# Optimization experiments

Hardware: AMD Instinct MI355X
Metric: run time of the kernel (lower is better)

Reference implementation:

```python
import jax, jax.numpy as jnp
import numpy as np

P2 = 8
BN_EPS = 1e-5


def _slice_maps(p2):
    # Faithfully reproduce the buggy fs[:, i*j-1] indexing: later loop
    # iterations overwrite earlier ones; slots never written stay zero.
    last = {}
    for i in range(1, p2 + 1):
        for j in range(1, p2 + 1):
            last[i * j - 1] = (i - 1, j - 1)
    src_i = np.zeros(p2 * p2, np.int32)
    src_j = np.zeros(p2 * p2, np.int32)
    mask = np.zeros(p2 * p2, np.float32)
    for k, (ii, jj) in last.items():
        src_i[k], src_j[k], mask[k] = ii, jj, 1.0
    # unslice: output patch (i,j) reads slot (i+1)*(j+1)-1
    uns = np.array([[(i + 1) * (j + 1) - 1 for j in range(p2)] for i in range(p2)], np.int32)
    return src_i, src_j, mask, uns


def setup_inputs() -> dict:
    key = jax.random.key(0)
    ks = jax.random.split(key, 16)
    C, N, p2 = 32, 8, P2
    s = 0.05
    inp = {
        "x": jax.random.normal(ks[0], (8, C, 512, 512), jnp.float32),
        "w30": jax.random.normal(ks[1], (N, C, 3, 3), jnp.float32) * s,
        "b30": jnp.zeros((N,), jnp.float32),
        "w10": jax.random.normal(ks[2], (C, C), jnp.float32) * s,
        "b10": jnp.zeros((C,), jnp.float32),
        "w11": jax.random.normal(ks[3], (N, N), jnp.float32) * s,
        "b11": jnp.zeros((N,), jnp.float32),
        "w12a": jax.random.normal(ks[4], (p2, p2 * p2), jnp.float32) * s,
        "b12a": jnp.zeros((p2,), jnp.float32),
        "w12b": jax.random.normal(ks[5], (p2, p2), jnp.float32) * s,
        "b12b": jnp.zeros((p2,), jnp.float32),
        "w12c": jax.random.normal(ks[6], (p2 * p2, p2), jnp.float32) * s,
        "b12c": jnp.zeros((p2 * p2,), jnp.float32),
        "w31": jax.random.normal(ks[7], (C, C), jnp.float32) * s,
        "b31": jnp.zeros((C,), jnp.float32),
        "bn_gamma": jnp.ones((C,), jnp.float32),
        "bn_beta": jnp.zeros((C,), jnp.float32),
        "bn_mean": jnp.zeros((C,), jnp.float32),
        "bn_var": jnp.ones((C,), jnp.float32),
    }
    return inp


def reference(x, w30, b30, w10, b10, w11, b11, w12a, b12a, w12b, b12b,
              w12c, b12c, w31, b31, bn_gamma, bn_beta, bn_mean, bn_var):
    p2 = P2
    b, C, H, W = x.shape
    h, wd = H // p2, W // p2
    L = h * wd
    N = w30.shape[0]
    src_i, src_j, mask_np, uns = _slice_maps(p2)

    # --- slice into patches (with the original's overwrite/zero semantics) ---
    patches = x.reshape(b, C, p2, h, p2, wd).transpose(0, 2, 4, 1, 3, 5)  # [b,p2,p2,C,h,w]
    fs = patches[:, src_i, src_j] * jnp.asarray(mask_np)[None, :, None, None, None]
    fs = fs.reshape(b * p2 * p2, C, h, wd)

    # --- graph_convolution ---
    B = jax.lax.conv_general_dilated(fs, w30, (1, 1), 'SAME',
            dimension_numbers=('NCHW', 'OIHW', 'NCHW')) + b30[None, :, None, None]
    B = jax.nn.relu(B)                                    # [bp, N, h, w]
    B1 = B.reshape(b * p2 * p2, N, L)
    fs1 = fs.reshape(b * p2 * p2, C, L)
    fs2 = jnp.einsum('bnl,bcl->bnc', B1, fs1)              # [bp, N, C]
    fs3 = jax.nn.relu(jnp.einsum('on,bnc->boc', w11, fs2) + b11[None, :, None])
    fs5 = jax.nn.relu(jnp.einsum('oc,bcn->bon', w10, fs3.transpose(0, 2, 1)) + b10[None, :, None])  # [bp,C,N]
    fs6 = jnp.einsum('bnl,bcn->bcl', B1, fs5)              # [bp, C, L]
    fs6 = fs6.reshape(b, p2 * p2, C, h, wd)

    fg = x.reshape(b, C, 8, H // 8, 8, W // 8).mean(axis=(3, 5))  # [b,C,8,8]
    fg1 = fg.reshape(b, C, p2 * p2).transpose(0, 2, 1)            # [b, p2^2, C]
    g = jax.nn.relu(jnp.einsum('ok,bkc->boc', w12a, fg1) + b12a[None, :, None])
    g = jax.nn.relu(jnp.einsum('ok,bkc->boc', w12b, g) + b12b[None, :, None])
    g = jax.nn.sigmoid(jnp.einsum('ok,bkc->boc', w12c, g) + b12c[None, :, None])  # [b,p2^2,C]
    out5 = g[:, :, :, None, None] * fs6                            # [b,p2^2,C,h,w]

    # --- unslice back to image (patch (i,j) reads slot (i+1)*(j+1)-1) ---
    gathered = out5[:, uns]                                        # [b,p2,p2,C,h,w]
    out = gathered.transpose(0, 3, 1, 4, 2, 5).reshape(b, C, H, W)

    # --- conv31: 1x1 conv + BatchNorm(eval) + ReLU, residual add ---
    y = jnp.einsum('oc,bchw->bohw', w31, out) + b31[None, :, None, None]
    y = (y - bn_mean[None, :, None, None]) * jax.lax.rsqrt(bn_var[None, :, None, None] + BN_EPS)
    y = jax.nn.relu(y * bn_gamma[None, :, None, None] + bn_beta[None, :, None, None])
    return y + x
```

## Files before the change

kernel.cpp:

```cpp
#include <hip/hip_runtime.h>
#include <math.h>
#include <stdint.h>

#define HW 512
#define NACT 30
#define NINACT 34

#define CONV_BLOCKS 1920
#define ZERO_BLOCKS 68
#define FG_BLOCKS   8704
#define KA_GRID (CONV_BLOCKS + ZERO_BLOCKS + FG_BLOCKS)

struct Maps {
    int src_i[64];
    int src_j[64];
    int mask[64];
    int aidx[64];
    int act_k[NACT];
    int inact_k[NINACT];
};

static Maps make_maps() {
    Maps m;
    for (int k = 0; k < 64; k++) { m.src_i[k]=0; m.src_j[k]=0; m.mask[k]=0; m.aidx[k]=-1; }
    for (int i = 1; i <= 8; i++)
        for (int j = 1; j <= 8; j++) {
            int k = i*j-1;
            m.src_i[k]=i-1; m.src_j[k]=j-1; m.mask[k]=1;
        }
    int cnt=0, icnt=0;
    for (int k=0;k<64;k++) {
        if (m.mask[k]) { m.aidx[k]=cnt; if (cnt < NACT) m.act_k[cnt]=k; cnt++; }
        else           { if (icnt < NINACT) m.inact_k[icnt]=k; icnt++; }
    }
    return m;
}

__global__ __launch_bounds__(256, 8) void k_A(
        const float* __restrict__ x, const float* __restrict__ w30,
        const float* __restrict__ b30, float* __restrict__ B,
        float* __restrict__ fgw, float* __restrict__ fs2g, Maps m) {
    int gid = blockIdx.x;
    int t = threadIdx.x;

    if (gid < CONV_BLOCKS) {
        int blk = gid >> 3;
        int rt  = gid & 7;
        int a = blk % NACT, b = blk / NACT;
        int k = m.act_k[a];
        int spi = m.src_i[k], spj = m.src_j[k];
        int r0 = rt*8;

        __shared__ float wlc[288];
        __shared__ __align__(16) float xs[4*10*72];

        for (int idx = t; idx < 4*10*72; idx += 256) xs[idx] = 0.f;

        int col = t & 63, tl = t >> 6;
        float acc[2][8];
        #pragma unroll
        for (int rr=0; rr<2; rr++)
            #pragma unroll
            for (int n=0;n<8;n++) acc[rr][n]=0.f;

        const float* xb = x + (size_t)b*32*HW*HW;

        for (int c0 = 0; c0 < 32; c0 += 4) {
            __syncthreads();
            for (int idx = t; idx < 288; idx += 256) {
                int cc = idx / 72;
                int rem = idx - cc*72;
                wlc[idx] = w30[((rem & 7)*32 + c0 + cc)*9 + (rem >> 3)];
            }
            for (int idx = t; idx < 640; idx += 256) {
                int cc = idx / 160;
                int rem = idx - cc*160;
                int r = rem >> 4;
                int q = rem & 15;
                int pr = r0 - 1 + r;
                float4 v = make_float4(0.f,0.f,0.f,0.f);
                if (pr >= 0 && pr < 64)
                    v = *(const float4*)(xb + (size_t)(c0+cc)*HW*HW + (size_t)(spi*64+pr)*HW + spj*64 + q*4);
                *(float4*)(xs + cc*720 + r*72 + 4 + q*4) = v;
            }
            __syncthreads();
            #pragma unroll
            for (int cc = 0; cc < 4; cc++) {
                const float* xrow = xs + cc*720 + (tl*2)*72 + 3 + col;
                const float* wb = wlc + cc*72;
                #pragma unroll
                for (int dy = 0; dy < 3; dy++) {
                    float xa0 = xrow[dy*72 + 0];
                    float xa1 = xrow[dy*72 + 1];
                    float xa2 = xrow[dy*72 + 2];
                    float xb0 = xrow[dy*72 + 72];
                    float xb1 = xrow[dy*72 + 73];
                    float xb2 = xrow[dy*72 + 74];
                    #pragma unroll
                    for (int dx = 0; dx < 3; dx++) {
                        float4 wa0 = *(const float4*)(wb + (dy*3+dx)*8);
                        float4 wa1 = *(const float4*)(wb + (dy*3+dx)*8 + 4);
                        float x0 = (dx==0) ? xa0 : ((dx==1) ? xa1 : xa2);
                        float x1 = (dx==0) ? xb0 : ((dx==1) ? xb1 : xb2);
                        acc[0][0] = fmaf(x0, wa0.x, acc[0][0]);
                        acc[0][1] = fmaf(x0, wa0.y, acc[0][1]);
                        acc[0][2] = fmaf(x0, wa0.z, acc[0][2]);
                        acc[0][3] = fmaf(x0, wa0.w, acc[0][3]);
                        acc[0][4] = fmaf(x0, wa1.x, acc[0][4]);
                        acc[0][5] = fmaf(x0, wa1.y, acc[0][5]);
                        acc[0][6] = fmaf(x0, wa1.z, acc[0][6]);
                        acc[0][7] = fmaf(x0, wa1.w, acc[0][7]);
                        acc[1][0] = fmaf(x1, wa0.x, acc[1][0]);
                        acc[1][1] = fmaf(x1, wa0.y, acc[1][1]);
                        acc[1][2] = fmaf(x1, wa0.z, acc[1][2]);
                        acc[1][3] = fmaf(x1, wa0.w, acc[1][3]);
                        acc[1][4] = fmaf(x1, wa1.x, acc[1][4]);
                        acc[1][5] = fmaf(x1, wa1.y, acc[1][5]);
                        acc[1][6] = fmaf(x1, wa1.z, acc[1][6]);
                        acc[1][7] = fmaf(x1, wa1.w, acc[1][7]);
                    }
                }
            }
        }
        float* Bp = B + (size_t)(b*NACT+a)*8*4096;
        #pragma unroll
        for (int rr=0; rr<2; rr++) {
            int y = r0 + tl*2 + rr;
            #pragma unroll
            for (int n=0;n<8;n++)
                Bp[n*4096 + y*64 + col] = fmaxf(acc[rr][n] + b30[n], 0.f);
        }
    } else if (gid < CONV_BLOCKS + ZERO_BLOCKS) {
        int z = gid - CONV_BLOCKS;
        if (z < 60) {
            float4* p = (float4*)(fs2g + z*1024);
            p[t] = make_float4(0.f,0.f,0.f,0.f);
        } else {
            int b = z - 60;
            for (int idx = t; idx < 960; idx += 256) {
                int a = idx >> 5, c = idx & 31;
                fgw[(b*64 + m.act_k[a])*32 + c] = 0.f;
            }
        }
    } else {
        int id = gid - CONV_BLOCKS - ZERO_BLOCKS;
        int q = id % NINACT;
        int bc = id / NINACT;
        int c = bc & 31;
        int b = bc >> 5;
        int k = m.inact_k[q];
        int pi = k >> 3, pj = k & 7;
        const float* xp = x + (size_t)(b*32+c)*HW*HW;
        float s = 0.f;
        #pragma unroll
        for (int ii = 0; ii < 4; ii++) {
            int idx4 = t + 256*ii;
            int y = idx4 >> 4;
            int xx = (idx4 & 15) * 4;
            float4 v = *(const float4*)(xp + (size_t)(pi*64 + y)*HW + pj*64 + xx);
            s += v.x + v.y + v.z + v.w;
        }
        for (int off = 32; off > 0; off >>= 1) s += __shfl_down(s, off);
        __shared__ float p[4];
        if ((t & 63) == 0) p[t >> 6] = s;
        __syncthreads();
        if (t == 0) {
            float tot = p[0]+p[1]+p[2]+p[3];
            fgw[(b*64 + k)*32 + c] = tot * (1.0f/4096.0f);
        }
    }
}

__global__ __launch_bounds__(256, 8) void k_fs2a(
        const float* __restrict__ x, const float* __restrict__ B,
        float* __restrict__ fs2g, float* __restrict__ fgw, Maps m) {
    int blk = blockIdx.x;
    int rt = blockIdx.y;
    int a = blk % NACT, b = blk / NACT;
    int k = m.act_k[a];
    int spi = m.src_i[k], spj = m.src_j[k];
    int l0 = rt*128;

    __shared__ __align__(16) float xs[32*132];

    int t = threadIdx.x;
    const float* xb = x + (size_t)b*32*HW*HW;
    #pragma unroll
    for (int q4 = 0; q4 < 4; q4++) {
        int idx = t + 256*q4;
        int c = idx >> 5, lq = idx & 31;
        int l = l0 + lq*4;
        int y = l >> 6, xx = l & 63;
        float4 v = *(const float4*)(xb + (size_t)c*HW*HW + (size_t)(spi*64+y)*HW + spj*64 + xx);
        *(float4*)(xs + c*132 + lq*4) = v;
    }
    __syncthreads();

    int n = t >> 5, c = t & 31;
    const float4* Bg4 = (const float4*)(B + (size_t)(b*NACT+a)*8*4096 + (size_t)n*4096 + l0);
    const float4* xs4 = (const float4*)(xs + c*132);
    float facc = 0.f;
    #pragma unroll 4
    for (int q = 0; q < 32; q++) {
        float4 bv = Bg4[q];
        float4 xv = xs4[q];
        facc = fmaf(bv.x, xv.x, facc);
        facc = fmaf(bv.y, xv.y, facc);
        facc = fmaf(bv.z, xv.z, facc);
        facc = fmaf(bv.w, xv.w, facc);
    }
    atomicAdd(&fs2g[(size_t)(b*NACT+a)*256 + n*32 + c], facc);

    if (t < 32) {
        const float4* xc4 = (const float4*)(xs + t*132);
        float s = 0.f;
        #pragma unroll 4
        for (int q = 0; q < 32; q++) {
            float4 v = xc4[q];
            s += v.x + v.y + v.z + v.w;
        }
        atomicAdd(&fgw[(b*64 + k)*32 + t], s * (1.0f/4096.0f));
    }
}

__global__ __launch_bounds__(256) void k_mid(
        const float* __restrict__ fs2g,
        const float* __restrict__ w11, const float* __restrict__ b11,
        const float* __restrict__ w10, const float* __restrict__ b10,
        float* __restrict__ fs5,
        const float* __restrict__ fgw,
        const float* __restrict__ w12a, const float* __restrict__ b12a,
        const float* __restrict__ w12b, const float* __restrict__ b12b,
        const float* __restrict__ w12c, const float* __restrict__ b12c,
        float* __restrict__ g, Maps m) {
    int gid = blockIdx.x;
    int t = threadIdx.x;
    if (gid < 240) {
        int a = gid % NACT, b = gid / NACT;
        int k = m.act_k[a];
        __shared__ float fs2s[8*33], fs3s[8*33];
        {
            int n = t >> 5, c = t & 31;
            fs2s[n*33+c] = fs2g[(size_t)(b*NACT+a)*256 + n*32 + c];
        }
        __syncthreads();
        {
            int o = t >> 5, c = t & 31;
            float v = b11[o];
            #pragma unroll
            for (int n=0;n<8;n++) v += w11[o*8+n]*fs2s[n*33+c];
            fs3s[o*33+c] = fmaxf(v, 0.f);
        }
        __syncthreads();
        {
            int cp = t >> 3, n = t & 7;
            float v = b10[cp];
            #pragma unroll
            for (int c=0;c<32;c++) v += w10[cp*32+c]*fs3s[n*33+c];
            fs5[((size_t)(b*64+k)*32 + cp)*8 + n] = fmaxf(v, 0.f);
        }
    } else {
        int b = gid - 240;
        int c = t;
        if (c >= 32) return;
        float fg[64];
        #pragma unroll
        for (int k = 0; k < 64; k++) fg[k] = fgw[(b*64+k)*32 + c];
        float g1[8], g2[8];
        #pragma unroll
        for (int o = 0; o < 8; o++) {
            float v = b12a[o];
            #pragma unroll
            for (int k2 = 0; k2 < 64; k2++) v += w12a[o*64+k2]*fg[k2];
            g1[o] = fmaxf(v, 0.f);
        }
        #pragma unroll
        for (int o = 0; o < 8; o++) {
            float v = b12b[o];
            #pragma unroll
            for (int k2 = 0; k2 < 8; k2++) v += w12b[o*8+k2]*g1[k2];
            g2[o] = fmaxf(v, 0.f);
        }
        for (int o = 0; o < 64; o++) {
            float v = b12c[o];
            #pragma unroll
            for (int k2 = 0; k2 < 8; k2++) v += w12c[o*8+k2]*g2[k2];
            g[(b*64+o)*32 + c] = 1.f / (1.f + expf(-v));
        }
    }
}

__global__ __launch_bounds__(256) void k_out(
        const float* __restrict__ x, const float* __restrict__ B,
        const float* __restrict__ fs5, const float* __restrict__ g,
        const float* __restrict__ w31, const float* __restrict__ b31,
        const float* __restrict__ gamma, const float* __restrict__ beta,
        const float* __restrict__ mean, const float* __restrict__ var,
        float* __restrict__ out, Maps m) {
    int blk = blockIdx.x;
    int rt = blockIdx.y;
    int h  = blockIdx.z;
    int ij = blk & 63, b = blk >> 6;
    int i = ij >> 3, j = ij & 7;
    int K = (i+1)*(j+1) - 1;
    int aK = m.aidx[K];
    __shared__ float Ms[128];
    __shared__ float ss2[16], sh2[16];
    int t = threadIdx.x;
    if (t < 128) {
        int ol = t >> 3, n = t & 7;
        int o = h*16 + ol;
        const float* f5 = fs5 + (size_t)(b*64+K)*32*8;
        const float* gg = g + (size_t)(b*64+K)*32;
        float v = 0.f;
        #pragma unroll
        for (int c=0;c<32;c++) v += w31[o*32+c]*gg[c]*f5[c*8+n];
        Ms[ol*8+n] = v;
    } else if (t < 144) {
        int ol = t - 128;
        int o = h*16 + ol;
        float sc = rsqrtf(var[o] + 1e-5f) * gamma[o];
        ss2[ol] = sc;
        sh2[ol] = (b31[o] - mean[o])*sc + beta[o];
    }
    __syncthreads();

    int hh = t >> 7;
    int gidx = t & 127;
    int r = gidx >> 4, q = gidx & 15;
    int y = rt*8 + r;
    int Y = i*64 + y;
    int X = j*64 + q*4;
    int obase = hh*8;
    const float* Bp = B + (size_t)(b*NACT+aK)*8*4096 + y*64 + q*4;
    const float* xb = x + ((size_t)(b*32 + h*16 + obase)*HW + Y)*HW + X;
    float* ob = out + ((size_t)(b*32 + h*16 + obase)*HW + Y)*HW + X;

    float4 Bv[8];
    #pragma unroll
    for (int n=0;n<8;n++) Bv[n] = *(const float4*)(Bp + n*4096);

    #pragma unroll 8
    for (int oo = 0; oo < 8; oo++) {
        int ol = obase + oo;
        float4 Ma = *(const float4*)(Ms + ol*8);
        float4 Mb = *(const float4*)(Ms + ol*8 + 4);
        float so = ss2[ol], ho = sh2[ol];
        float4 xv = *(const float4*)(xb + (size_t)oo*HW*HW);
        float4 yv;
        yv.x = Bv[0].x*Ma.x + Bv[1].x*Ma.y + Bv[2].x*Ma.z + Bv[3].x*Ma.w
             + Bv[4].x*Mb.x + Bv[5].x*Mb.y + Bv[6].x*Mb.z + Bv[7].x*Mb.w;
        yv.y = Bv[0].y*Ma.x + Bv[1].y*Ma.y + Bv[2].y*Ma.z + Bv[3].y*Ma.w
             + Bv[4].y*Mb.x + Bv[5].y*Mb.y + Bv[6].y*Mb.z + Bv[7].y*Mb.w;
        yv.z = Bv[0].z*Ma.x + Bv[1].z*Ma.y + Bv[2].z*Ma.z + Bv[3].z*Ma.w
             + Bv[4].z*Mb.x + Bv[5].z*Mb.y + Bv[6].z*Mb.z + Bv[7].z*Mb.w;
        yv.w = Bv[0].w*Ma.x + Bv[1].w*Ma.y + Bv[2].w*Ma.z + Bv[3].w*Ma.w
             + Bv[4].w*Mb.x + Bv[5].w*Mb.y + Bv[6].w*Mb.z + Bv[7].w*Mb.w;
        float4 res;
        res.x = fmaxf(yv.x*so + ho, 0.f) + xv.x;
        res.y = fmaxf(yv.y*so + ho, 0.f) + xv.y;
        res.z = fmaxf(yv.z*so + ho, 0.f) + xv.z;
        res.w = fmaxf(yv.w*so + ho, 0.f) + xv.w;
        *(float4*)(ob + (size_t)oo*HW*HW) = res;
    }
}

extern "C" void kernel_launch(void* const* d_in, const int* in_sizes, int n_in,
                              void* d_out, int out_size, void* d_ws, size_t ws_size,
                              hipStream_t stream) {
    const float* x    = (const float*)d_in[0];
    const float* w30  = (const float*)d_in[1];
    const float* b30  = (const float*)d_in[2];
    const float* w10  = (const float*)d_in[3];
    const float* b10  = (const float*)d_in[4];
    const float* w11  = (const float*)d_in[5];
    const float* b11  = (const float*)d_in[6];
    const float* w12a = (const float*)d_in[7];
    const float* b12a = (const float*)d_in[8];
    const float* w12b = (const float*)d_in[9];
    const float* b12b = (const float*)d_in[10];
    const float* w12c = (const float*)d_in[11];
    const float* b12c = (const float*)d_in[12];
    const float* w31  = (const float*)d_in[13];
    const float* b31  = (const float*)d_in[14];
    const float* gam  = (const float*)d_in[15];
    const float* bet  = (const float*)d_in[16];
    const float* mea  = (const float*)d_in[17];
    const float* var  = (const float*)d_in[18];
    float* out = (float*)d_out;

    float* ws   = (float*)d_ws;
    float* B    = ws;
    float* fs5  = B + 7864320;
    float* fgw  = fs5 + 131072;
    float* g    = fgw + 16384;
    float* fs2g = g + 16384;

    static Maps m = make_maps();

    k_A   <<<dim3(KA_GRID),   256, 0, stream>>>(x, w30, b30, B, fgw, fs2g, m);
    k_fs2a<<<dim3(240, 32),   256, 0, stream>>>(x, B, fs2g, fgw, m);
    k_mid <<<dim3(248),       256, 0, stream>>>(fs2g, w11, b11, w10, b10, fs5,
                                                fgw, w12a, b12a, w12b, b12b, w12c, b12c, g, m);
    k_out <<<dim3(512, 8, 2), 256, 0, stream>>>(x, B, fs5, g, w31, b31, gam, bet, mea, var, out, m);
}
```

Baseline: 615.4 us.

## Fuse mid-stage MLPs into output kernel, recomputing per block

Removes the k_mid kernel launch and its fs5/g workspace round-trip. Each k_out block now recomputes the conv11/conv10 channel mixing for its patch and the ADP_weight MLP for its slot, keeping the results in shared memory. This saves a launch and a small global write/read. In exchange, 8192 blocks redundantly run the 64x8 MLP plus extra syncs before the bandwidth-bound output phase. The MLP work runs on only 32 threads per block.

```diff
diff --git a/kernel.cpp b/kernel.cpp
--- a/kernel.cpp
+++ b/kernel.cpp
@@ -223,76 +223,14 @@
     }
 }
 
-__global__ __launch_bounds__(256) void k_mid(
-        const float* __restrict__ fs2g,
+__global__ __launch_bounds__(256) void k_out(
+        const float* __restrict__ x, const float* __restrict__ B,
+        const float* __restrict__ fs2g, const float* __restrict__ fgw,
         const float* __restrict__ w11, const float* __restrict__ b11,
         const float* __restrict__ w10, const float* __restrict__ b10,
-        float* __restrict__ fs5,
-        const float* __restrict__ fgw,
         const float* __restrict__ w12a, const float* __restrict__ b12a,
         const float* __restrict__ w12b, const float* __restrict__ b12b,
         const float* __restrict__ w12c, const float* __restrict__ b12c,
-        float* __restrict__ g, Maps m) {
-    int gid = blockIdx.x;
-    int t = threadIdx.x;
-    if (gid < 240) {
-        int a = gid % NACT, b = gid / NACT;
-        int k = m.act_k[a];
-        __shared__ float fs2s[8*33], fs3s[8*33];
-        {
-            int n = t >> 5, c = t & 31;
-            fs2s[n*33+c] = fs2g[(size_t)(b*NACT+a)*256 + n*32 + c];
-        }
-        __syncthreads();
-        {
-            int o = t >> 5, c = t & 31;
-            float v = b11[o];
-            #pragma unroll
-            for (int n=0;n<8;n++) v += w11[o*8+n]*fs2s[n*33+c];
-            fs3s[o*33+c] = fmaxf(v, 0.f);
-        }
-        __syncthreads();
-        {
-            int cp = t >> 3, n = t & 7;
-            float v = b10[cp];
-            #pragma unroll
-            for (int c=0;c<32;c++) v += w10[cp*32+c]*fs3s[n*33+c];
-            fs5[((size_t)(b*64+k)*32 + cp)*8 + n] = fmaxf(v, 0.f);
-        }
-    } else {
-        int b = gid - 240;
-        int c = t;
-        if (c >= 32) return;
-        float fg[64];
-        #pragma unroll
-        for (int k = 0; k < 64; k++) fg[k] = fgw[(b*64+k)*32 + c];
-        float g1[8], g2[8];
-        #pragma unroll
-        for (int o = 0; o < 8; o++) {
-            float v = b12a[o];
-            #pragma unroll
-            for (int k2 = 0; k2 < 64; k2++) v += w12a[o*64+k2]*fg[k2];
-            g1[o] = fmaxf(v, 0.f);
-        }
-        #pragma unroll
-        for (int o = 0; o < 8; o++) {
-            float v = b12b[o];
-            #pragma unroll
-            for (int k2 = 0; k2 < 8; k2++) v += w12b[o*8+k2]*g1[k2];
-            g2[o] = fmaxf(v, 0.f);
-        }
-        for (int o = 0; o < 64; o++) {
-            float v = b12c[o];
-            #pragma unroll
-            for (int k2 = 0; k2 < 8; k2++) v += w12c[o*8+k2]*g2[k2];
-            g[(b*64+o)*32 + c] = 1.f / (1.f + expf(-v));
-        }
-    }
-}
-
-__global__ __launch_bounds__(256) void k_out(
-        const float* __restrict__ x, const float* __restrict__ B,
-        const float* __restrict__ fs5, const float* __restrict__ g,
         const float* __restrict__ w31, const float* __restrict__ b31,
         const float* __restrict__ gamma, const float* __restrict__ beta,
         const float* __restrict__ mean, const float* __restrict__ var,
@@ -304,24 +242,74 @@
     int i = ij >> 3, j = ij & 7;
     int K = (i+1)*(j+1) - 1;
     int aK = m.aidx[K];
+
+    __shared__ float fs2s[8*33];
+    __shared__ float fs3s[8*33];
+    __shared__ float fs5s[32*8];
+    __shared__ float gs[32];
     __shared__ float Ms[128];
     __shared__ float ss2[16], sh2[16];
     int t = threadIdx.x;
-    if (t < 128) {
-        int ol = t >> 3, n = t & 7;
-        int o = h*16 + ol;
-        const float* f5 = fs5 + (size_t)(b*64+K)*32*8;
-        const float* gg = g + (size_t)(b*64+K)*32;
-        float v = 0.f;
-        #pragma unroll
-        for (int c=0;c<32;c++) v += w31[o*32+c]*gg[c]*f5[c*8+n];
-        Ms[ol*8+n] = v;
-    } else if (t < 144) {
+
+    {
+        int n = t >> 5, c = t & 31;
+        fs2s[n*33+c] = fs2g[(size_t)(b*NACT+aK)*256 + n*32 + c];
+    }
+    __syncthreads();
+    {
+        int o = t >> 5, c = t & 31;
+        float v = b11[o];
+        #pragma unroll
+        for (int n=0;n<8;n++) v += w11[o*8+n]*fs2s[n*33+c];
+        fs3s[o*33+c] = fmaxf(v, 0.f);
+    }
+    __syncthreads();
+    {
+        int cp = t >> 3, n = t & 7;
+        float v = b10[cp];
+        #pragma unroll
+        for (int c=0;c<32;c++) v += w10[cp*32+c]*fs3s[n*33+c];
+        fs5s[cp*8+n] = fmaxf(v, 0.f);
+    }
+    if (t < 32) {
+        int c = t;
+        float fg[64];
+        #pragma unroll
+        for (int k = 0; k < 64; k++) fg[k] = fgw[(b*64+k)*32 + c];
+        float g1[8], g2[8];
+        #pragma unroll
+        for (int o = 0; o < 8; o++) {
+            float v = b12a[o];
+            #pragma unroll
+            for (int k2 = 0; k2 < 64; k2++) v += w12a[o*64+k2]*fg[k2];
+            g1[o] = fmaxf(v, 0.f);
+        }
+        #pragma unroll
+        for (int o = 0; o < 8; o++) {
+            float v = b12b[o];
+            #pragma unroll
+            for (int k2 = 0; k2 < 8; k2++) v += w12b[o*8+k2]*g1[k2];
+            g2[o] = fmaxf(v, 0.f);
+        }
+        float v = b12c[K];
+        #pragma unroll
+        for (int k2 = 0; k2 < 8; k2++) v += w12c[K*8+k2]*g2[k2];
+        gs[c] = 1.f / (1.f + expf(-v));
+    } else if (t >= 128 && t < 144) {
         int ol = t - 128;
         int o = h*16 + ol;
         float sc = rsqrtf(var[o] + 1e-5f) * gamma[o];
         ss2[ol] = sc;
         sh2[ol] = (b31[o] - mean[o])*sc + beta[o];
+    }
+    __syncthreads();
+    if (t < 128) {
+        int ol = t >> 3, n = t & 7;
+        int o = h*16 + ol;
+        float v = 0.f;
+        #pragma unroll
+        for (int c=0;c<32;c++) v += w31[o*32+c]*gs[c]*fs5s[c*8+n];
+        Ms[ol*8+n] = v;
     }
     __syncthreads();
 
@@ -391,16 +379,15 @@
 
     float* ws   = (float*)d_ws;
     float* B    = ws;
-    float* fs5  = B + 7864320;
-    float* fgw  = fs5 + 131072;
-    float* g    = fgw + 16384;
-    float* fs2g = g + 16384;
+    float* fgw  = B + 7864320;
+    float* fs2g = fgw + 16384;
 
     static Maps m = make_maps();
 
     k_A   <<<dim3(KA_GRID),   256, 0, stream>>>(x, w30, b30, B, fgw, fs2g, m);
     k_fs2a<<<dim3(240, 32),   256, 0, stream>>>(x, B, fs2g, fgw, m);
-    k_mid <<<dim3(248),       256, 0, stream>>>(fs2g, w11, b11, w10, b10, fs5,
-                                                fgw, w12a, b12a, w12b, b12b, w12c, b12c, g, m);
-    k_out <<<dim3(512, 8, 2), 256, 0, stream>>>(x, B, fs5, g, w31, b31, gam, bet, mea, var, out, m);
-}
+    k_out <<<dim3(512, 8, 2), 256, 0, stream>>>(x, B, fs2g, fgw,
+                                                w11, b11, w10, b10,
+                                                w12a, b12a, w12b, b12b, w12c, b12c,
+                                                w31, b31, gam, bet, mea, var, out, m);
+}
```

New measurement: 604.5 us, median of 2. Within noise of the previous version (-1.8%).
